# Kernel tuning notes

Hardware: AMD Instinct MI355X
Metric: run time of the kernel (lower is better)

The kernel has to match this reference:

```python
import jax, jax.numpy as jnp
import numpy as np

# module constants (from init_kwargs)
R_EQ = 1.0
WELL_DEPTH = 1.0
CUTOFF = 2.5
HEAL = 0.5

N_EDGES = 20_000_000
N_ATOMS = 1_000_000
N_MOL = 1000


def setup_inputs() -> dict:
    key = jax.random.key(0)
    k1, k2 = jax.random.split(key)
    vec_ij = jax.random.normal(k1, (N_EDGES, 3), dtype=jnp.float32)
    positions = jax.random.normal(k2, (N_ATOMS, 3), dtype=jnp.float32)
    idx_i = jax.random.randint(jax.random.fold_in(key, 1), (N_EDGES,), 0, N_ATOMS, dtype=jnp.int32)
    # sorted molecule indices covering [0, N_MOL), last element == N_MOL-1
    idx_m = (jnp.arange(N_ATOMS, dtype=jnp.int32) * N_MOL // N_ATOMS).astype(jnp.int32)
    return {"vec_ij": vec_ij, "positions": positions, "idx_i": idx_i, "idx_m": idx_m}


def reference(vec_ij, positions, idx_i, idx_m):
    # per-edge distance [E,1]
    r = jnp.linalg.norm(vec_ij, axis=1, keepdims=True)
    # CustomCutoff switching function
    t = (r - (CUTOFF - HEAL)) / HEAL
    r_function = 1.0 + t * t * (2.0 * t - 3.0)
    switch = jnp.where(r > CUTOFF - HEAL, r_function, jnp.ones_like(r))
    switch = jnp.where(r > CUTOFF, jnp.zeros_like(r), switch)
    # LJ pair energy
    power_6 = (R_EQ / r) ** 6
    power_12 = power_6 * power_6
    yij = (power_12 - power_6) * switch  # [E,1]
    # scatter-add edges -> atoms
    yi = jax.ops.segment_sum(yij, idx_i, num_segments=positions.shape[0])  # [N,1]
    # index-add atoms -> molecules
    y = jax.ops.segment_sum(yi, idx_m, num_segments=N_MOL)  # [M,1]
    y = jnp.squeeze(y, -1)
    return WELL_DEPTH * 0.5 * y
```

## Files before the change

kernel.cpp:

```cpp
#include <hip/hip_runtime.h>

#define RCUT2  6.25f
#define RIN2   4.0f
#define BT     512
#define EPT    4
#define TILE   (BT*EPT)
#define VTB    (TILE*12)
#define WSB    (VTB/8)
#define NB     768
#define RB     256
#define RCHUNK 8


__global__ __launch_bounds__(256) void init_k(float* __restrict__ out, int n_mol,
                                              int* __restrict__ flag, int flag_init) {
    int i = blockIdx.x * 256 + threadIdx.x;
    if (i < n_mol) out[i] = 0.0f;
    if (i == 0) *flag = flag_init;
}

__global__ __launch_bounds__(256) void build_bounds(
    const int* __restrict__ idx_m, int* __restrict__ start,
    int* __restrict__ flag, int n_atoms, int n_mol) {
    int a = blockIdx.x * 256 + threadIdx.x;
    if (a >= n_atoms) return;
    int m  = idx_m[a];
    int pm = (a == 0) ? -1 : idx_m[a - 1];
    for (int mm = pm + 1; mm <= m; ++mm) start[mm] = a;
    if (a == n_atoms - 1)
        for (int mm = m + 1; mm <= n_mol; ++mm) start[mm] = n_atoms;
    int mf = (int)(((unsigned long long)(unsigned)a * (unsigned)n_mol) / (unsigned)n_atoms);
    if (m != mf) atomicAnd(flag, 0);
}


__device__ __forceinline__ void lj_body(
    float vx, float vy, float vz, int a,
    bool uni, const int* __restrict__ bounds_g, float* bins,
    int n_mol, unsigned long long M, int sh)
{
    float r2 = fmaf(vx, vx, fmaf(vy, vy, vz * vz));
    if (r2 > RCUT2) return;
    float inv2 = __builtin_amdgcn_rcpf(r2);
    float p6   = inv2 * inv2 * inv2;
    float y    = fmaf(p6, p6, -p6);
    float r  = __builtin_amdgcn_sqrtf(r2);
    float t  = fmaf(2.0f, r, -4.0f);
    float sw = fmaf(t * t, fmaf(2.0f, t, -3.0f), 1.0f);
    y *= (r2 > RIN2) ? sw : 1.0f;
    unsigned q = (unsigned)a * (unsigned)n_mol;
    int m = (int)(((unsigned long long)q * M) >> sh);
    if (!uni) {
        if (m > n_mol - 1) m = n_mol - 1;
        if (m < 0) m = 0;
        while (m > 0 && a < bounds_g[m]) --m;
        while (m < n_mol - 1 && a >= bounds_g[m + 1]) ++m;
    }
    atomicAdd(&bins[m], y);
}

__device__ __forceinline__ void gload_lds16(const void* g, void* l) {
    __builtin_amdgcn_global_load_lds(
        (__attribute__((address_space(1))) void*)g,
        (__attribute__((address_space(3))) void*)l,
        16, 0, 0);
}


__global__ __launch_bounds__(BT) void lj_staged(
    const float* __restrict__ vec,
    const int*   __restrict__ idx_i,
    const int*   __restrict__ bounds_g,
    const int*   __restrict__ flag,
    float*       __restrict__ dest,
    int n_edges, int n_mol, int bins_pad,
    unsigned long long M, int sh, int use_partial)
{
    extern __shared__ char smem[];
    float* bins = (float*)smem;
    char* sb0 = smem + bins_pad;
    char* sb1 = sb0 + VTB;
    for (int i = threadIdx.x; i < n_mol; i += BT) bins[i] = 0.0f;
    const bool uni = (*flag != 0);

    const int ntiles = n_edges / TILE;
    const int gdim   = (int)gridDim.x;
    const char* vecb = (const char*)vec;
    const int w    = threadIdx.x >> 6;
    const int lane = threadIdx.x & 63;

    if ((int)blockIdx.x < ntiles) {
        const char* g = vecb + (size_t)blockIdx.x * VTB + (size_t)(w * WSB + lane * 16);
        char* l = sb0 + w * WSB;
        #pragma unroll
        for (int op = 0; op < 3; ++op)
            gload_lds16(g + op * 1024, l + op * 1024);
    }

    int cur = 0;
    for (int t = blockIdx.x; t < ntiles; t += gdim) {
        __syncthreads();

        int tn = t + gdim;
        if (tn < ntiles) {
            const char* g = vecb + (size_t)tn * VTB + (size_t)(w * WSB + lane * 16);
            char* l = (cur ? sb0 : sb1) + w * WSB;
            #pragma unroll
            for (int op = 0; op < 3; ++op)
                gload_lds16(g + op * 1024, l + op * 1024);
        }

        const float* vb = (const float*)(cur ? sb1 : sb0);
        const size_t eb = (size_t)t * TILE;
        const int l0 = threadIdx.x;
        int a0 = idx_i[eb + l0];
        int a1 = idx_i[eb + l0 + BT];
        int a2 = idx_i[eb + l0 + 2 * BT];
        int a3 = idx_i[eb + l0 + 3 * BT];
        float x0 = vb[3 * l0 + 0],            y0 = vb[3 * l0 + 1],            z0 = vb[3 * l0 + 2];
        float x1 = vb[3 * (l0 + BT) + 0],     y1 = vb[3 * (l0 + BT) + 1],     z1 = vb[3 * (l0 + BT) + 2];
        float x2 = vb[3 * (l0 + 2 * BT) + 0], y2 = vb[3 * (l0 + 2 * BT) + 1], z2 = vb[3 * (l0 + 2 * BT) + 2];
        float x3 = vb[3 * (l0 + 3 * BT) + 0], y3 = vb[3 * (l0 + 3 * BT) + 1], z3 = vb[3 * (l0 + 3 * BT) + 2];
        lj_body(x0, y0, z0, a0, uni, bounds_g, bins, n_mol, M, sh);
        lj_body(x1, y1, z1, a1, uni, bounds_g, bins, n_mol, M, sh);
        lj_body(x2, y2, z2, a2, uni, bounds_g, bins, n_mol, M, sh);
        lj_body(x3, y3, z3, a3, uni, bounds_g, bins, n_mol, M, sh);
        cur ^= 1;
    }

    if (blockIdx.x == 0) {
        for (int e = ntiles * TILE + (int)threadIdx.x; e < n_edges; e += BT) {
            size_t b = 3 * (size_t)e;
            lj_body(vec[b], vec[b + 1], vec[b + 2], idx_i[e],
                    uni, bounds_g, bins, n_mol, M, sh);
        }
    }

    __syncthreads();
    if (use_partial) {
        float* myp = dest + (size_t)blockIdx.x * (size_t)n_mol;
        for (int i = threadIdx.x; i < n_mol; i += BT) myp[i] = bins[i];
    } else {
        unsigned off = (blockIdx.x * 131u) % (unsigned)n_mol;
        for (int i = threadIdx.x; i < n_mol; i += BT) {
            int j = i + (int)off; if (j >= n_mol) j -= n_mol;
            float bv = bins[j];
            if (bv != 0.0f) atomicAdd(&dest[j], 0.5f * bv);
        }
    }
}

__global__ __launch_bounds__(BT) void lj_fallback(
    const float* __restrict__ vec, const int* __restrict__ idx_i,
    const int* __restrict__ bounds_g, const int* __restrict__ flag,
    float* __restrict__ dest, int n_edges, int n_mol,
    unsigned long long M, int sh, int use_partial)
{
    extern __shared__ float bins[];
    for (int i = threadIdx.x; i < n_mol; i += BT) bins[i] = 0.0f;
    const bool uni = (*flag != 0);
    __syncthreads();
    const int stride = gridDim.x * BT;
    for (int e = blockIdx.x * BT + threadIdx.x; e < n_edges; e += stride) {
        size_t b = 3 * (size_t)e;
        lj_body(vec[b], vec[b + 1], vec[b + 2], idx_i[e],
                uni, bounds_g, bins, n_mol, M, sh);
    }
    __syncthreads();
    if (use_partial) {
        float* myp = dest + (size_t)blockIdx.x * (size_t)n_mol;
        for (int i = threadIdx.x; i < n_mol; i += BT) myp[i] = bins[i];
    } else {
        unsigned off = (blockIdx.x * 131u) % (unsigned)n_mol;
        for (int i = threadIdx.x; i < n_mol; i += BT) {
            int j = i + (int)off; if (j >= n_mol) j -= n_mol;
            float bv = bins[j];
            if (bv != 0.0f) atomicAdd(&dest[j], 0.5f * bv);
        }
    }
}

__global__ __launch_bounds__(RB) void reduce_k(
    const float* __restrict__ partial, float* __restrict__ out,
    int n_mol, int nb)
{
    const int colblocks = (n_mol + RB - 1) / RB;
    const int cb = blockIdx.x % colblocks;
    const int ch = blockIdx.x / colblocks;
    const int j  = cb * RB + (int)threadIdx.x;
    if (j >= n_mol) return;
    const int rows = nb / RCHUNK;
    const int b0 = ch * rows, b1 = b0 + rows;
    float s = 0.0f;
    #pragma unroll 4
    for (int b = b0; b < b1; ++b) s += partial[(size_t)b * (size_t)n_mol + j];
    atomicAdd(&out[j], 0.5f * s);
}


extern "C" void kernel_launch(void* const* d_in, const int* in_sizes, int n_in,
                              void* d_out, int out_size, void* d_ws, size_t ws_size,
                              hipStream_t stream) {
    const float* vec   = (const float*)d_in[0];
    const int*   idx_i = (const int*)d_in[2];
    const int*   idx_m = (const int*)d_in[3];
    float*       out   = (float*)d_out;

    const int n_edges = in_sizes[2];
    const int n_atoms = in_sizes[3];
    const int n_mol   = out_size;

    const size_t partial_bytes = (size_t)NB * (size_t)n_mol * sizeof(float);
    const size_t need = partial_bytes + (size_t)(n_mol + 2) * sizeof(int);
    const int use_partial = (ws_size >= need) ? 1 : 0;

    float* partial;
    int*   start;
    if (use_partial) {
        partial = (float*)d_ws;
        start   = (int*)(partial + (size_t)NB * (size_t)n_mol);
    } else {
        partial = nullptr;
        start   = (int*)d_ws;
    }
    int* flag = start + (n_mol + 1);

    unsigned d = (unsigned)n_atoms;
    unsigned long long M = 1; int sh = 32;
    bool ok = ((unsigned long long)(unsigned)n_mol * d) <= 0x7fffffffull;
    if (ok) {
        bool found = false;
        for (sh = 32; sh <= 62; ++sh) {
            unsigned long long tk = 1ull << sh;
            M = tk / d + 1;
            unsigned long long e = M * d - tk;
            if (e <= (1ull << (sh - 31))) { found = true; break; }
        }
        ok = found;
    }
    if (!ok) { M = 0; sh = 0; }

    init_k<<<(n_mol + 255) / 256, 256, 0, stream>>>(out, n_mol, flag, ok ? 1 : 0);
    build_bounds<<<(n_atoms + 255) / 256, 256, 0, stream>>>(idx_m, start, flag, n_atoms, n_mol);

    const int    bins_pad = (n_mol * 4 + 255) & ~255;
    const size_t lds_staged = (size_t)bins_pad + 2 * VTB;

    if (lds_staged <= 64 * 1024) {
        lj_staged<<<NB, BT, lds_staged, stream>>>(
            vec, idx_i, start, flag,
            use_partial ? partial : out,
            n_edges, n_mol, bins_pad, M, sh, use_partial);
    } else {
        lj_fallback<<<NB, BT, (size_t)n_mol * sizeof(float), stream>>>(
            vec, idx_i, start, flag,
            use_partial ? partial : out,
            n_edges, n_mol, M, sh, use_partial);
    }

    if (use_partial) {
        const int colblocks = (n_mol + RB - 1) / RB;
        reduce_k<<<colblocks * RCHUNK, RB, 0, stream>>>(partial, out, n_mol, NB);
    }
}
```

Measured before the change: 412.0 us.

## Vectorize edge loads, prefetch indices, and drop partial-sum reduction kernel

Each thread now handles four consecutive edges, reading its indices as one int4 and its 12 floats as three float4 LDS reads. The index load for the next tile is issued one iteration ahead, alongside the async LDS copy. The per-block partial buffer and the separate reduce kernel are removed, so every block atomically adds its LDS bins straight into the output. This saves one kernel launch and the partial traffic, at the cost of 768 blocks contending with atomics on about 1000 outputs.

```diff
diff --git a/kernel.cpp b/kernel.cpp
--- a/kernel.cpp
+++ b/kernel.cpp
@@ -8,8 +8,6 @@
 #define VTB    (TILE*12)
 #define WSB    (VTB/8)
 #define NB     768
-#define RB     256
-#define RCHUNK 8
 
 
 __global__ __launch_bounds__(256) void init_k(float* __restrict__ out, int n_mol,
@@ -72,9 +70,9 @@
     const int*   __restrict__ idx_i,
     const int*   __restrict__ bounds_g,
     const int*   __restrict__ flag,
-    float*       __restrict__ dest,
+    float*       __restrict__ out,
     int n_edges, int n_mol, int bins_pad,
-    unsigned long long M, int sh, int use_partial)
+    unsigned long long M, int sh)
 {
     extern __shared__ char smem[];
     float* bins = (float*)smem;
@@ -85,51 +83,52 @@
 
     const int ntiles = n_edges / TILE;
     const int gdim   = (int)gridDim.x;
+    const int tid    = (int)threadIdx.x;
+    const int w      = tid >> 6;
+    const int lane   = tid & 63;
     const char* vecb = (const char*)vec;
-    const int w    = threadIdx.x >> 6;
-    const int lane = threadIdx.x & 63;
-
-    if ((int)blockIdx.x < ntiles) {
-        const char* g = vecb + (size_t)blockIdx.x * VTB + (size_t)(w * WSB + lane * 16);
+    const int4* idx4 = (const int4*)idx_i;
+
+    int4 ia = make_int4(0, 0, 0, 0);
+    const int t0 = (int)blockIdx.x;
+    if (t0 < ntiles) {
+        const char* g = vecb + (size_t)t0 * VTB + (size_t)(w * WSB + lane * 16);
         char* l = sb0 + w * WSB;
         #pragma unroll
         for (int op = 0; op < 3; ++op)
             gload_lds16(g + op * 1024, l + op * 1024);
+        ia = idx4[(size_t)t0 * (TILE / 4) + tid];
     }
 
     int cur = 0;
-    for (int t = blockIdx.x; t < ntiles; t += gdim) {
+    for (int t = t0; t < ntiles; t += gdim) {
         __syncthreads();
 
         int tn = t + gdim;
+        int4 ian = make_int4(0, 0, 0, 0);
         if (tn < ntiles) {
             const char* g = vecb + (size_t)tn * VTB + (size_t)(w * WSB + lane * 16);
             char* l = (cur ? sb0 : sb1) + w * WSB;
             #pragma unroll
             for (int op = 0; op < 3; ++op)
                 gload_lds16(g + op * 1024, l + op * 1024);
+            ian = idx4[(size_t)tn * (TILE / 4) + tid];
         }
 
-        const float* vb = (const float*)(cur ? sb1 : sb0);
-        const size_t eb = (size_t)t * TILE;
-        const int l0 = threadIdx.x;
-        int a0 = idx_i[eb + l0];
-        int a1 = idx_i[eb + l0 + BT];
-        int a2 = idx_i[eb + l0 + 2 * BT];
-        int a3 = idx_i[eb + l0 + 3 * BT];
-        float x0 = vb[3 * l0 + 0],            y0 = vb[3 * l0 + 1],            z0 = vb[3 * l0 + 2];
-        float x1 = vb[3 * (l0 + BT) + 0],     y1 = vb[3 * (l0 + BT) + 1],     z1 = vb[3 * (l0 + BT) + 2];
-        float x2 = vb[3 * (l0 + 2 * BT) + 0], y2 = vb[3 * (l0 + 2 * BT) + 1], z2 = vb[3 * (l0 + 2 * BT) + 2];
-        float x3 = vb[3 * (l0 + 3 * BT) + 0], y3 = vb[3 * (l0 + 3 * BT) + 1], z3 = vb[3 * (l0 + 3 * BT) + 2];
-        lj_body(x0, y0, z0, a0, uni, bounds_g, bins, n_mol, M, sh);
-        lj_body(x1, y1, z1, a1, uni, bounds_g, bins, n_mol, M, sh);
-        lj_body(x2, y2, z2, a2, uni, bounds_g, bins, n_mol, M, sh);
-        lj_body(x3, y3, z3, a3, uni, bounds_g, bins, n_mol, M, sh);
+        const float4* vb4 = (const float4*)(cur ? sb1 : sb0);
+        float4 w0 = vb4[3 * tid + 0];
+        float4 w1 = vb4[3 * tid + 1];
+        float4 w2 = vb4[3 * tid + 2];
+        lj_body(w0.x, w0.y, w0.z, ia.x, uni, bounds_g, bins, n_mol, M, sh);
+        lj_body(w0.w, w1.x, w1.y, ia.y, uni, bounds_g, bins, n_mol, M, sh);
+        lj_body(w1.z, w1.w, w2.x, ia.z, uni, bounds_g, bins, n_mol, M, sh);
+        lj_body(w2.y, w2.z, w2.w, ia.w, uni, bounds_g, bins, n_mol, M, sh);
+        ia = ian;
         cur ^= 1;
     }
 
     if (blockIdx.x == 0) {
-        for (int e = ntiles * TILE + (int)threadIdx.x; e < n_edges; e += BT) {
+        for (int e = ntiles * TILE + tid; e < n_edges; e += BT) {
             size_t b = 3 * (size_t)e;
             lj_body(vec[b], vec[b + 1], vec[b + 2], idx_i[e],
                     uni, bounds_g, bins, n_mol, M, sh);
@@ -137,24 +136,19 @@
     }
 
     __syncthreads();
-    if (use_partial) {
-        float* myp = dest + (size_t)blockIdx.x * (size_t)n_mol;
-        for (int i = threadIdx.x; i < n_mol; i += BT) myp[i] = bins[i];
-    } else {
-        unsigned off = (blockIdx.x * 131u) % (unsigned)n_mol;
-        for (int i = threadIdx.x; i < n_mol; i += BT) {
-            int j = i + (int)off; if (j >= n_mol) j -= n_mol;
-            float bv = bins[j];
-            if (bv != 0.0f) atomicAdd(&dest[j], 0.5f * bv);
-        }
+    unsigned off = (blockIdx.x * 131u) % (unsigned)n_mol;
+    for (int i = tid; i < n_mol; i += BT) {
+        int j = i + (int)off; if (j >= n_mol) j -= n_mol;
+        float bv = bins[j];
+        if (bv != 0.0f) atomicAdd(&out[j], 0.5f * bv);
     }
 }
 
 __global__ __launch_bounds__(BT) void lj_fallback(
     const float* __restrict__ vec, const int* __restrict__ idx_i,
     const int* __restrict__ bounds_g, const int* __restrict__ flag,
-    float* __restrict__ dest, int n_edges, int n_mol,
-    unsigned long long M, int sh, int use_partial)
+    float* __restrict__ out, int n_edges, int n_mol,
+    unsigned long long M, int sh)
 {
     extern __shared__ float bins[];
     for (int i = threadIdx.x; i < n_mol; i += BT) bins[i] = 0.0f;
@@ -167,34 +161,12 @@
                 uni, bounds_g, bins, n_mol, M, sh);
     }
     __syncthreads();
-    if (use_partial) {
-        float* myp = dest + (size_t)blockIdx.x * (size_t)n_mol;
-        for (int i = threadIdx.x; i < n_mol; i += BT) myp[i] = bins[i];
-    } else {
-        unsigned off = (blockIdx.x * 131u) % (unsigned)n_mol;
-        for (int i = threadIdx.x; i < n_mol; i += BT) {
-            int j = i + (int)off; if (j >= n_mol) j -= n_mol;
-            float bv = bins[j];
-            if (bv != 0.0f) atomicAdd(&dest[j], 0.5f * bv);
-        }
-    }
-}
-
-__global__ __launch_bounds__(RB) void reduce_k(
-    const float* __restrict__ partial, float* __restrict__ out,
-    int n_mol, int nb)
-{
-    const int colblocks = (n_mol + RB - 1) / RB;
-    const int cb = blockIdx.x % colblocks;
-    const int ch = blockIdx.x / colblocks;
-    const int j  = cb * RB + (int)threadIdx.x;
-    if (j >= n_mol) return;
-    const int rows = nb / RCHUNK;
-    const int b0 = ch * rows, b1 = b0 + rows;
-    float s = 0.0f;
-    #pragma unroll 4
-    for (int b = b0; b < b1; ++b) s += partial[(size_t)b * (size_t)n_mol + j];
-    atomicAdd(&out[j], 0.5f * s);
+    unsigned off = (blockIdx.x * 131u) % (unsigned)n_mol;
+    for (int i = threadIdx.x; i < n_mol; i += BT) {
+        int j = i + (int)off; if (j >= n_mol) j -= n_mol;
+        float bv = bins[j];
+        if (bv != 0.0f) atomicAdd(&out[j], 0.5f * bv);
+    }
 }
 
 
@@ -210,20 +182,8 @@
     const int n_atoms = in_sizes[3];
     const int n_mol   = out_size;
 
-    const size_t partial_bytes = (size_t)NB * (size_t)n_mol * sizeof(float);
-    const size_t need = partial_bytes + (size_t)(n_mol + 2) * sizeof(int);
-    const int use_partial = (ws_size >= need) ? 1 : 0;
-
-    float* partial;
-    int*   start;
-    if (use_partial) {
-        partial = (float*)d_ws;
-        start   = (int*)(partial + (size_t)NB * (size_t)n_mol);
-    } else {
-        partial = nullptr;
-        start   = (int*)d_ws;
-    }
-    int* flag = start + (n_mol + 1);
+    int* start = (int*)d_ws;
+    int* flag  = (int*)d_ws + (n_mol + 2);
 
     unsigned d = (unsigned)n_atoms;
     unsigned long long M = 1; int sh = 32;
@@ -243,23 +203,14 @@
     init_k<<<(n_mol + 255) / 256, 256, 0, stream>>>(out, n_mol, flag, ok ? 1 : 0);
     build_bounds<<<(n_atoms + 255) / 256, 256, 0, stream>>>(idx_m, start, flag, n_atoms, n_mol);
 
-    const int    bins_pad = (n_mol * 4 + 255) & ~255;
+    const int    bins_pad   = (n_mol * 4 + 255) & ~255;
     const size_t lds_staged = (size_t)bins_pad + 2 * VTB;
 
     if (lds_staged <= 64 * 1024) {
         lj_staged<<<NB, BT, lds_staged, stream>>>(
-            vec, idx_i, start, flag,
-            use_partial ? partial : out,
-            n_edges, n_mol, bins_pad, M, sh, use_partial);
+            vec, idx_i, start, flag, out, n_edges, n_mol, bins_pad, M, sh);
     } else {
         lj_fallback<<<NB, BT, (size_t)n_mol * sizeof(float), stream>>>(
-            vec, idx_i, start, flag,
-            use_partial ? partial : out,
-            n_edges, n_mol, M, sh, use_partial);
-    }
-
-    if (use_partial) {
-        const int colblocks = (n_mol + RB - 1) / RB;
-        reduce_k<<<colblocks * RCHUNK, RB, 0, stream>>>(partial, out, n_mol, NB);
-    }
-}
+            vec, idx_i, start, flag, out, n_edges, n_mol, M, sh);
+    }
+}
```

Result: no change. 410.8 us (-0.3%).
